# Kernel tuning notes

Measured on AMD Instinct MI355X. Metric: run time of the kernel, lower is better.

Reference implementation:

```python
import jax, jax.numpy as jnp
import numpy as np

B, C_IN, H, W = 4, 128, 32, 128   # W must equal out_channels (fc_out acts on last dim)
C_OUT, NUM_HEADS = 128, 2
BN_EPS = 1e-5


def setup_inputs() -> dict:
    key = jax.random.key(0)
    ks = jax.random.split(key, 14)
    s = 0.05  # small init scale for weights
    d = {
        "x": jax.random.normal(ks[0], (B, C_IN, H, W), jnp.float32),
        "wq": jax.random.normal(ks[1], (C_OUT, C_IN), jnp.float32) * s,
        "bq": jax.random.normal(ks[2], (C_OUT,), jnp.float32) * s,
        "wk": jax.random.normal(ks[3], (C_OUT, C_IN), jnp.float32) * s,
        "bk": jax.random.normal(ks[4], (C_OUT,), jnp.float32) * s,
        "wv": jax.random.normal(ks[5], (C_OUT, C_IN), jnp.float32) * s,
        "bv": jax.random.normal(ks[6], (C_OUT,), jnp.float32) * s,
        "fc_w": jax.random.normal(ks[7], (C_OUT, C_OUT), jnp.float32) * s,
        "fc_b": jax.random.normal(ks[8], (C_OUT,), jnp.float32) * s,
        "bn_gamma": jnp.ones((C_OUT,), jnp.float32),
        "bn_beta": jnp.zeros((C_OUT,), jnp.float32),
        "bn_mean": jax.random.normal(ks[9], (C_OUT,), jnp.float32) * 0.1,
        "bn_var": jax.random.uniform(ks[10], (C_OUT,), jnp.float32, 0.5, 1.5),
        "prelu_a": jnp.full((1,), 0.25, jnp.float32),
    }
    return d


def reference(x, wq, bq, wk, bk, wv, bv, fc_w, fc_b,
              bn_gamma, bn_beta, bn_mean, bn_var, prelu_a):
    b, c_in, h, w = x.shape
    c_out = wq.shape[0]
    nh = NUM_HEADS
    dk = c_out // nh
    L = h * w
    xf = x.reshape(b, c_in, L)                                # (B, Cin, L)
    # 1x1 convs == per-token linear projections
    q = jnp.einsum('oi,bil->bol', wq, xf) + bq[:, None]       # (B, Cout, L)
    k = jnp.einsum('oi,bil->bol', wk, xf) + bk[:, None]
    v = jnp.einsum('oi,bil->bol', wv, xf) + bv[:, None]
    Q = q.reshape(b, nh, dk, L)                               # (B, h, d_k, L)
    K = k.reshape(b, nh, dk, L)
    V = v.reshape(b, nh, dk, L)
    # scaled dot-product attention over the L = H*W tokens
    scores = jnp.einsum('bhdl,bhdm->bhlm', Q, K) / jnp.sqrt(jnp.float32(dk))
    attn = jax.nn.softmax(scores, axis=-1)                    # (B, h, L, L)
    out = jnp.einsum('bhlm,bhdm->bhdl', attn, V)              # (B, h, d_k, L)
    out = out.reshape(b, c_out, h, w)                         # (B, Cout, H, W)
    # fc_out: torch Linear on the LAST dim (W == Cout)
    y = jnp.einsum('bchw,ow->bcho', out, fc_w) + fc_b         # (B, Cout, H, W)
    # BatchNorm2d (eval mode: running stats) over channel dim
    inv = jax.lax.rsqrt(bn_var + BN_EPS)
    y = (y - bn_mean[None, :, None, None]) * (inv * bn_gamma)[None, :, None, None] \
        + bn_beta[None, :, None, None]
    # PReLU (single shared slope); dropout is identity in eval
    y = jnp.where(y > 0, y, prelu_a[0] * y)
    return y
```

## Files before the change

### kernel.cpp

```cpp
#include <hip/hip_runtime.h>

typedef _Float16 f16x8 __attribute__((ext_vector_type(8)));
typedef _Float16 f16x4t __attribute__((ext_vector_type(4)));
typedef __fp16 h16x2 __attribute__((ext_vector_type(2)));
typedef float f32x4 __attribute__((ext_vector_type(4)));
typedef float f32x16 __attribute__((ext_vector_type(16)));

#define L_SZ 4096

__device__ __forceinline__ unsigned short f2h(float f) {
    _Float16 h = (_Float16)f;
    return __builtin_bit_cast(unsigned short, h);
}
__device__ __forceinline__ unsigned int pk2(float a, float b) {
    h16x2 p = __builtin_amdgcn_cvt_pkrtz(a, b);
    return __builtin_bit_cast(unsigned int, p);
}

#define SLOT(row, ci) ((((ci) * 64) + ((row) & 32) + (((row) & 31) ^ (ci))) * 8)

__global__ __launch_bounds__(256, 1) void qkv_kernel(
    const float* __restrict__ x,
    const float* __restrict__ wq, const float* __restrict__ bq,
    const float* __restrict__ wk, const float* __restrict__ bk,
    const float* __restrict__ wv, const float* __restrict__ bv,
    unsigned short* __restrict__ Qp, unsigned short* __restrict__ Kp,
    unsigned short* __restrict__ Vp)
{
    int blk = blockIdx.x;
    int bidx = blk >> 6;
    int l0 = (blk & 63) * 64;
    int tid = threadIdx.x;
    int wave = tid >> 6, lane = tid & 63;
    int c = lane & 15, qd = lane >> 4;

    __shared__ __align__(16) unsigned short Ws[384 * 128];
    __shared__ __align__(16) unsigned short Sc[9216];

    #pragma unroll
    for (int t = 0; t < 96; ++t) {
        int e2 = tid + t * 256;
        const float* src = (e2 < 8192) ? wq : (e2 < 16384 ? wk : wv);
        int eo = (e2 * 2) & 16383;
        float2 v = *(const float2*)&src[eo];
        int e = e2 * 2;
        int o = e >> 7, ci = (e & 127) >> 3, j = e & 7;
        *(unsigned int*)&Ws[o * 128 + ((ci ^ (o & 15)) * 8) + j] = pk2(v.x, v.y);
    }

    unsigned short* Xs = Sc;
    #pragma unroll
    for (int it = 0; it < 8; ++it) {
        int i  = (tid >> 4) + 16 * it;
        int l4 = (tid & 15) * 4;
        const float4 v = *(const float4*)&x[(bidx * 128 + i) * L_SZ + l0 + l4];
        float vv[4] = {v.x, v.y, v.z, v.w};
        int ci = i >> 3;
        #pragma unroll
        for (int u = 0; u < 4; ++u) {
            int l = l4 + u;
            Xs[l * 128 + ((ci ^ (l & 15)) * 8) + (i & 7)] = f2h(vv[u]);
        }
    }
    __syncthreads();

    f16x8 afrag[4];
    #pragma unroll
    for (int kc = 0; kc < 4; ++kc) {
        int l = wave * 16 + c;
        int ci = kc * 4 + qd;
        afrag[kc] = *(const f16x8*)&Xs[l * 128 + ((ci ^ (l & 15)) * 8)];
    }
    __syncthreads();

    f32x4 acc[24];
    #pragma unroll
    for (int nt = 0; nt < 24; ++nt) acc[nt] = (f32x4){0.f, 0.f, 0.f, 0.f};

    #pragma unroll
    for (int kc = 0; kc < 4; ++kc) {
        #pragma unroll
        for (int nt = 0; nt < 24; ++nt) {
            int o = nt * 16 + c;
            f16x8 bfrag = *(const f16x8*)&Ws[o * 128 + (((kc * 4 + qd) ^ c) * 8)];
            acc[nt] = __builtin_amdgcn_mfma_f32_16x16x32_f16(afrag[kc], bfrag, acc[nt], 0, 0, 0);
        }
    }

    unsigned short* Vt = Sc;
    const float s_q = 0.18033688011f;
    #pragma unroll
    for (int nt = 0; nt < 24; ++nt) {
        int p = nt >> 3;
        int o = (nt & 7) * 16 + c;
        int h = o >> 6, d = o & 63;
        #pragma unroll
        for (int r = 0; r < 4; ++r) {
            int ll = wave * 16 + qd * 4 + r;
            int l = l0 + ll;
            float val = acc[nt][r];
            if (p == 0) {
                val = (val + bq[o]) * s_q;
                Qp[((bidx * 2 + h) * L_SZ + l) * 64 + d] = f2h(val);
            } else if (p == 1) {
                val += bk[o];
                Kp[((bidx * 2 + h) * L_SZ + l) * 64 + d] = f2h(val);
            } else {
                val += bv[o];
                Vt[o * 72 + ll] = f2h(val);
            }
        }
    }
    __syncthreads();
    #pragma unroll
    for (int t = 0; t < 2; ++t) {
        int u = tid + t * 256;
        int row = u >> 2;
        int lc = (u & 3) * 16;
        uint4 a0 = *(const uint4*)&Vt[row * 72 + lc];
        uint4 a1 = *(const uint4*)&Vt[row * 72 + lc + 8];
        *(uint4*)&Vp[(size_t)(bidx * 128 + row) * L_SZ + l0 + lc] = a0;
        *(uint4*)&Vp[(size_t)(bidx * 128 + row) * L_SZ + l0 + lc + 8] = a1;
    }
}

__global__ __launch_bounds__(256, 3) void attn_kernel(
    const unsigned short* __restrict__ Qp, const unsigned short* __restrict__ Kp,
    const unsigned short* __restrict__ Vp,
    unsigned short* __restrict__ Opart, float* __restrict__ Mpart, float* __restrict__ Lpart)
{
    int blk = blockIdx.x;
    int lt = blk & 31;
    int bh = (blk >> 5) & 7;
    int sp = blk >> 8;
    int l0 = lt * 128;
    int tid = threadIdx.x;
    int wave = tid >> 6, lane = tid & 63;
    int ln = lane & 31, hi = lane >> 5;
    int b = bh >> 1, h = bh & 1;

    __shared__ __align__(16) unsigned short Ks[2][4096];
    __shared__ __align__(16) unsigned short Vs[2][4096];
    __shared__ __align__(16) unsigned short Ps[4][2048];

    const unsigned short* Qb = Qp + (size_t)bh * L_SZ * 64;
    const unsigned short* Kb = Kp + (size_t)bh * L_SZ * 64;
    const unsigned short* Vb = Vp + ((size_t)b * 128 + h * 64) * L_SZ;

    int lq = l0 + wave * 32 + ln;
    f16x8 qf[4];
    #pragma unroll
    for (int kc = 0; kc < 4; ++kc)
        qf[kc] = *(const f16x8*)&Qb[(size_t)lq * 64 + kc * 16 + hi * 8];

    float m_st = -1e30f, lsum = 0.f;
    f32x16 acc0 = {}, acc1 = {};

    int urow = tid >> 3, uci = tid & 7;
    int mglob = sp * 1024;

    uint4 kreg[2], vreg[2];
    #pragma unroll
    for (int j = 0; j < 2; ++j) {
        int row = urow + j * 32;
        kreg[j] = *(const uint4*)&Kb[(size_t)(mglob + row) * 64 + uci * 8];
        vreg[j] = *(const uint4*)&Vb[(size_t)row * L_SZ + mglob + uci * 8];
    }
    #pragma unroll
    for (int j = 0; j < 2; ++j) {
        int row = urow + j * 32;
        *(uint4*)&Ks[0][SLOT(row, uci)] = kreg[j];
        *(uint4*)&Vs[0][SLOT(row, uci)] = vreg[j];
    }

    for (int it = 0; it < 16; ++it) {
        int cur = it & 1;
        __syncthreads();
        if (it < 15) {
            int m0 = mglob + (it + 1) * 64;
            #pragma unroll
            for (int j = 0; j < 2; ++j) {
                int row = urow + j * 32;
                kreg[j] = *(const uint4*)&Kb[(size_t)(m0 + row) * 64 + uci * 8];
                vreg[j] = *(const uint4*)&Vb[(size_t)row * L_SZ + m0 + uci * 8];
            }
        }

        f32x16 s0 = {}, s1 = {};
        #pragma unroll
        for (int kc = 0; kc < 4; ++kc) {
            int cd = kc * 2 + hi;
            f16x8 k0 = *(const f16x8*)&Ks[cur][SLOT(ln, cd)];
            f16x8 k1 = *(const f16x8*)&Ks[cur][SLOT(32 + ln, cd)];
            s0 = __builtin_amdgcn_mfma_f32_32x32x16_f16(k0, qf[kc], s0, 0, 0, 0);
            s1 = __builtin_amdgcn_mfma_f32_32x32x16_f16(k1, qf[kc], s1, 0, 0, 0);
        }

        float mx = s0[0];
        #pragma unroll
        for (int r = 1; r < 16; ++r) mx = fmaxf(mx, s0[r]);
        #pragma unroll
        for (int r = 0; r < 16; ++r) mx = fmaxf(mx, s1[r]);
        mx = fmaxf(mx, __shfl_xor(mx, 32));
        float mnew = fmaxf(m_st, mx);
        float alpha = exp2f(m_st - mnew);
        m_st = mnew;
        float rsum = 0.f;
        #pragma unroll
        for (int r = 0; r < 16; ++r) { float p = exp2f(s0[r] - mnew); s0[r] = p; rsum += p; }
        #pragma unroll
        for (int r = 0; r < 16; ++r) { float p = exp2f(s1[r] - mnew); s1[r] = p; rsum += p; }
        lsum = lsum * alpha + rsum;
        #pragma unroll
        for (int r = 0; r < 16; ++r) { acc0[r] *= alpha; acc1[r] *= alpha; }

        #pragma unroll
        for (int g = 0; g < 4; ++g) {
            uint2 w0;
            w0.x = pk2(s0[g * 4 + 0], s0[g * 4 + 1]);
            w0.y = pk2(s0[g * 4 + 2], s0[g * 4 + 3]);
            *(uint2*)&Ps[wave][(g * 32 + (ln ^ g)) * 8 + hi * 4] = w0;
            int g2 = 4 + g;
            uint2 w1;
            w1.x = pk2(s1[g * 4 + 0], s1[g * 4 + 1]);
            w1.y = pk2(s1[g * 4 + 2], s1[g * 4 + 3]);
            *(uint2*)&Ps[wave][(g2 * 32 + (ln ^ g2)) * 8 + hi * 4] = w1;
        }

        #pragma unroll
        for (int kc = 0; kc < 4; ++kc) {
            int cd = kc * 2 + hi;
            f16x8 pf = *(const f16x8*)&Ps[wave][(cd * 32 + (ln ^ cd)) * 8];
            f16x8 v0 = *(const f16x8*)&Vs[cur][SLOT(ln, cd)];
            f16x8 v1 = *(const f16x8*)&Vs[cur][SLOT(32 + ln, cd)];
            acc0 = __builtin_amdgcn_mfma_f32_32x32x16_f16(v0, pf, acc0, 0, 0, 0);
            acc1 = __builtin_amdgcn_mfma_f32_32x32x16_f16(v1, pf, acc1, 0, 0, 0);
        }

        if (it < 15) {
            #pragma unroll
            for (int j = 0; j < 2; ++j) {
                int row = urow + j * 32;
                *(uint4*)&Ks[cur ^ 1][SLOT(row, uci)] = kreg[j];
                *(uint4*)&Vs[cur ^ 1][SLOT(row, uci)] = vreg[j];
            }
        }
    }

    float l_tot = lsum + __shfl_xor(lsum, 32);
    unsigned short* Ow = Opart + (size_t)(sp * 8 + bh) * 64 * 4096;
    #pragma unroll
    for (int r = 0; r < 16; ++r) {
        int d0 = (r & 3) + 8 * (r >> 2) + 4 * hi;
        Ow[(size_t)d0 * 4096 + lq] = f2h(acc0[r]);
        Ow[(size_t)(32 + d0) * 4096 + lq] = f2h(acc1[r]);
    }
    if (hi == 0) {
        Mpart[(sp * 8 + bh) * 4096 + lq] = m_st;
        Lpart[(sp * 8 + bh) * 4096 + lq] = l_tot;
    }
}

__global__ __launch_bounds__(256, 1) void fc_kernel(
    const unsigned short* __restrict__ Opart, const float* __restrict__ Mp,
    const float* __restrict__ Lp, const float* __restrict__ fcw_f,
    const float* __restrict__ fc_b, const float* __restrict__ bn_g,
    const float* __restrict__ bn_b, const float* __restrict__ bn_m,
    const float* __restrict__ bn_v, const float* __restrict__ prelu_a,
    float* __restrict__ out)
{
    int blk = blockIdx.x;
    int r0 = blk * 64;
    int tid = threadIdx.x;
    int c0 = (r0 >> 5) & 127;
    int bh = (r0 >> 12) * 2 + (c0 >> 6);

    __shared__ __align__(16) unsigned short Fw[128 * 128];
    __shared__ __align__(16) unsigned short SclU[4096 * 4];

    #pragma unroll
    for (int t = 0; t < 16; ++t) {
        int l = tid + t * 256;
        float m0 = Mp[(0 * 8 + bh) * 4096 + l], m1 = Mp[(1 * 8 + bh) * 4096 + l];
        float m2 = Mp[(2 * 8 + bh) * 4096 + l], m3 = Mp[(3 * 8 + bh) * 4096 + l];
        float mx = fmaxf(fmaxf(m0, m1), fmaxf(m2, m3));
        float a0 = exp2f(m0 - mx), a1 = exp2f(m1 - mx);
        float a2 = exp2f(m2 - mx), a3 = exp2f(m3 - mx);
        float den = a0 * Lp[(0 * 8 + bh) * 4096 + l] + a1 * Lp[(1 * 8 + bh) * 4096 + l]
                  + a2 * Lp[(2 * 8 + bh) * 4096 + l] + a3 * Lp[(3 * 8 + bh) * 4096 + l];
        float inv = 1.0f / den;
        int hh = l >> 7, ww = l & 127;
        int slot = hh * 128 + ((ww + hh) & 127);
        uint2 sc;
        sc.x = pk2(a0 * inv, a1 * inv);
        sc.y = pk2(a2 * inv, a3 * inv);
        *(uint2*)&SclU[slot * 4] = sc;
    }
    #pragma unroll
    for (int t = 0; t < 32; ++t) {
        int e2 = tid + t * 256;
        float2 v = *(const float2*)&fcw_f[e2 * 2];
        int e = e2 * 2;
        int o = e >> 7, ci = (e & 127) >> 3, j = e & 7;
        *(unsigned int*)&Fw[o * 128 + ((ci ^ (o & 15)) * 8) + j] = pk2(v.x, v.y);
    }
    __syncthreads();

    int wave = tid >> 6, lane = tid & 63;
    int c = lane & 15, qd = lane >> 4;
    int rw = r0 + wave * 16;
    int row = rw + c;
    int ch = (row >> 5) & 127, hh = row & 31, d = ch & 63;

    f16x8 af[4];
    #pragma unroll
    for (int kc = 0; kc < 4; ++kc) {
        int w0 = kc * 32 + qd * 8;
        f16x8 ov[4];
        #pragma unroll
        for (int s = 0; s < 4; ++s)
            ov[s] = *(const f16x8*)&Opart[(size_t)(s * 8 + bh) * 262144 + (size_t)d * 4096 + hh * 128 + w0];
        #pragma unroll
        for (int j = 0; j < 8; ++j) {
            int slot = hh * 128 + ((w0 + j + hh) & 127);
            f16x4t sc = *(const f16x4t*)&SclU[slot * 4];
            float v = (float)ov[0][j] * (float)sc[0] + (float)ov[1][j] * (float)sc[1]
                    + (float)ov[2][j] * (float)sc[2] + (float)ov[3][j] * (float)sc[3];
            af[kc][j] = (_Float16)v;
        }
    }

    f32x4 acc[8];
    #pragma unroll
    for (int nt = 0; nt < 8; ++nt) acc[nt] = (f32x4){0.f, 0.f, 0.f, 0.f};
    #pragma unroll
    for (int kc = 0; kc < 4; ++kc) {
        #pragma unroll
        for (int nt = 0; nt < 8; ++nt) {
            int o = nt * 16 + c;
            f16x8 bf = *(const f16x8*)&Fw[o * 128 + (((kc * 4 + qd) ^ c) * 8)];
            acc[nt] = __builtin_amdgcn_mfma_f32_16x16x32_f16(af[kc], bf, acc[nt], 0, 0, 0);
        }
    }

    float pa = prelu_a[0];
    #pragma unroll
    for (int r = 0; r < 4; ++r) {
        int orow = rw + qd * 4 + r;
        int chn = (orow >> 5) & 127;
        float g  = bn_g[chn] * rsqrtf(bn_v[chn] + 1e-5f);
        float mn = bn_m[chn], bt = bn_b[chn];
        #pragma unroll
        for (int nt = 0; nt < 8; ++nt) {
            int o = nt * 16 + c;
            float y = (acc[nt][r] + fc_b[o] - mn) * g + bt;
            y = y > 0.f ? y : pa * y;
            out[(size_t)orow * 128 + o] = y;
        }
    }
}

extern "C" void kernel_launch(void* const* d_in, const int* in_sizes, int n_in,
                              void* d_out, int out_size, void* d_ws, size_t ws_size,
                              hipStream_t stream) {
    const float* x     = (const float*)d_in[0];
    const float* wq    = (const float*)d_in[1];
    const float* bq    = (const float*)d_in[2];
    const float* wk    = (const float*)d_in[3];
    const float* bk    = (const float*)d_in[4];
    const float* wv    = (const float*)d_in[5];
    const float* bv    = (const float*)d_in[6];
    const float* fcw_f = (const float*)d_in[7];
    const float* fcb   = (const float*)d_in[8];
    const float* bn_g  = (const float*)d_in[9];
    const float* bn_b  = (const float*)d_in[10];
    const float* bn_m  = (const float*)d_in[11];
    const float* bn_v  = (const float*)d_in[12];
    const float* pa    = (const float*)d_in[13];
    float* out = (float*)d_out;

    unsigned short* Qp  = (unsigned short*)d_ws;
    unsigned short* Kp  = Qp + 8 * L_SZ * 64;
    unsigned short* Vp  = Kp + 8 * L_SZ * 64;
    unsigned short* Opart = Vp + 8 * L_SZ * 64;
    float* Mpart = (float*)(Opart + 4 * 8 * 64 * L_SZ);
    float* Lpart = Mpart + 4 * 8 * L_SZ;

    hipLaunchKernelGGL(qkv_kernel,  dim3(256),  dim3(256), 0, stream,
                       x, wq, bq, wk, bk, wv, bv, Qp, Kp, Vp);
    hipLaunchKernelGGL(attn_kernel, dim3(1024), dim3(256), 0, stream,
                       Qp, Kp, Vp, Opart, Mpart, Lpart);
    hipLaunchKernelGGL(fc_kernel,   dim3(256),  dim3(256), 0, stream,
                       Opart, Mpart, Lpart, fcw_f, fcb, bn_g, bn_b, bn_m, bn_v, pa, out);
}
```

Before: 170.1 us.

## Split QKV and FC work across more blocks, single-buffer attention LDS, lazy rescale

```diff
diff --git a/kernel.cpp b/kernel.cpp
--- a/kernel.cpp
+++ b/kernel.cpp
@@ -16,10 +16,18 @@
     h16x2 p = __builtin_amdgcn_cvt_pkrtz(a, b);
     return __builtin_bit_cast(unsigned int, p);
 }
+__device__ __forceinline__ f16x8 ld8f(const float* __restrict__ p) {
+    float4 a = *(const float4*)p;
+    float4 b = *(const float4*)(p + 4);
+    uint4 u;
+    u.x = pk2(a.x, a.y); u.y = pk2(a.z, a.w);
+    u.z = pk2(b.x, b.y); u.w = pk2(b.z, b.w);
+    return __builtin_bit_cast(f16x8, u);
+}
 
 #define SLOT(row, ci) ((((ci) * 64) + ((row) & 32) + (((row) & 31) ^ (ci))) * 8)
 
-__global__ __launch_bounds__(256, 1) void qkv_kernel(
+__global__ __launch_bounds__(256) void qkv_kernel(
     const float* __restrict__ x,
     const float* __restrict__ wq, const float* __restrict__ bq,
     const float* __restrict__ wk, const float* __restrict__ bk,
@@ -28,27 +36,20 @@
     unsigned short* __restrict__ Vp)
 {
     int blk = blockIdx.x;
-    int bidx = blk >> 6;
-    int l0 = (blk & 63) * 64;
+    int proj = blk >> 8;
+    int rem = blk & 255;
+    int bidx = rem >> 6;
+    int l0 = (rem & 63) * 64;
     int tid = threadIdx.x;
     int wave = tid >> 6, lane = tid & 63;
     int c = lane & 15, qd = lane >> 4;
 
-    __shared__ __align__(16) unsigned short Ws[384 * 128];
-    __shared__ __align__(16) unsigned short Sc[9216];
-
-    #pragma unroll
-    for (int t = 0; t < 96; ++t) {
-        int e2 = tid + t * 256;
-        const float* src = (e2 < 8192) ? wq : (e2 < 16384 ? wk : wv);
-        int eo = (e2 * 2) & 16383;
-        float2 v = *(const float2*)&src[eo];
-        int e = e2 * 2;
-        int o = e >> 7, ci = (e & 127) >> 3, j = e & 7;
-        *(unsigned int*)&Ws[o * 128 + ((ci ^ (o & 15)) * 8) + j] = pk2(v.x, v.y);
-    }
-
-    unsigned short* Xs = Sc;
+    const float* W   = (proj == 0) ? wq : (proj == 1 ? wk : wv);
+    const float* bia = (proj == 0) ? bq : (proj == 1 ? bk : bv);
+
+    __shared__ __align__(16) unsigned short Sh[8448];
+
+    unsigned short* Xs = Sh;
     #pragma unroll
     for (int it = 0; it < 8; ++it) {
         int i  = (tid >> 4) + 16 * it;
@@ -73,58 +74,64 @@
     }
     __syncthreads();
 
-    f32x4 acc[24];
-    #pragma unroll
-    for (int nt = 0; nt < 24; ++nt) acc[nt] = (f32x4){0.f, 0.f, 0.f, 0.f};
+    f32x4 acc[8];
+    #pragma unroll
+    for (int nt = 0; nt < 8; ++nt) acc[nt] = (f32x4){0.f, 0.f, 0.f, 0.f};
 
     #pragma unroll
     for (int kc = 0; kc < 4; ++kc) {
         #pragma unroll
-        for (int nt = 0; nt < 24; ++nt) {
+        for (int nt = 0; nt < 8; ++nt) {
             int o = nt * 16 + c;
-            f16x8 bfrag = *(const f16x8*)&Ws[o * 128 + (((kc * 4 + qd) ^ c) * 8)];
+            f16x8 bfrag = ld8f(&W[o * 128 + kc * 32 + qd * 8]);
             acc[nt] = __builtin_amdgcn_mfma_f32_16x16x32_f16(afrag[kc], bfrag, acc[nt], 0, 0, 0);
         }
     }
 
-    unsigned short* Vt = Sc;
     const float s_q = 0.18033688011f;
-    #pragma unroll
-    for (int nt = 0; nt < 24; ++nt) {
-        int p = nt >> 3;
-        int o = (nt & 7) * 16 + c;
-        int h = o >> 6, d = o & 63;
-        #pragma unroll
-        for (int r = 0; r < 4; ++r) {
-            int ll = wave * 16 + qd * 4 + r;
-            int l = l0 + ll;
-            float val = acc[nt][r];
-            if (p == 0) {
-                val = (val + bq[o]) * s_q;
-                Qp[((bidx * 2 + h) * L_SZ + l) * 64 + d] = f2h(val);
-            } else if (p == 1) {
-                val += bk[o];
-                Kp[((bidx * 2 + h) * L_SZ + l) * 64 + d] = f2h(val);
-            } else {
-                val += bv[o];
-                Vt[o * 72 + ll] = f2h(val);
+    if (proj < 2) {
+        unsigned short* dst = (proj == 0) ? Qp : Kp;
+        #pragma unroll
+        for (int nt = 0; nt < 8; ++nt) {
+            int o = nt * 16 + c;
+            int h = o >> 6, d = o & 63;
+            float bo = bia[o];
+            #pragma unroll
+            for (int r = 0; r < 4; ++r) {
+                int l = l0 + wave * 16 + qd * 4 + r;
+                float val = acc[nt][r] + bo;
+                if (proj == 0) val *= s_q;
+                dst[((bidx * 2 + h) * L_SZ + l) * 64 + d] = f2h(val);
             }
         }
-    }
-    __syncthreads();
-    #pragma unroll
-    for (int t = 0; t < 2; ++t) {
-        int u = tid + t * 256;
-        int row = u >> 2;
-        int lc = (u & 3) * 16;
-        uint4 a0 = *(const uint4*)&Vt[row * 72 + lc];
-        uint4 a1 = *(const uint4*)&Vt[row * 72 + lc + 8];
-        *(uint4*)&Vp[(size_t)(bidx * 128 + row) * L_SZ + l0 + lc] = a0;
-        *(uint4*)&Vp[(size_t)(bidx * 128 + row) * L_SZ + l0 + lc + 8] = a1;
-    }
-}
-
-__global__ __launch_bounds__(256, 3) void attn_kernel(
+    } else {
+        unsigned short* Vt = Sh;
+        #pragma unroll
+        for (int nt = 0; nt < 8; ++nt) {
+            int o = nt * 16 + c;
+            float bo = bia[o];
+            #pragma unroll
+            for (int r = 0; r < 4; ++r) {
+                int ll = wave * 16 + qd * 4 + r;
+                Vt[o * 66 + ll] = f2h(acc[nt][r] + bo);
+            }
+        }
+        __syncthreads();
+        int row = tid >> 1;
+        int seg = (tid & 1) * 32;
+        #pragma unroll
+        for (int k = 0; k < 4; ++k) {
+            uint4 a;
+            a.x = *(unsigned int*)&Vt[row * 66 + seg + k * 8 + 0];
+            a.y = *(unsigned int*)&Vt[row * 66 + seg + k * 8 + 2];
+            a.z = *(unsigned int*)&Vt[row * 66 + seg + k * 8 + 4];
+            a.w = *(unsigned int*)&Vt[row * 66 + seg + k * 8 + 6];
+            *(uint4*)&Vp[(size_t)(bidx * 128 + row) * L_SZ + l0 + seg + k * 8] = a;
+        }
+    }
+}
+
+__global__ __launch_bounds__(256, 4) void attn_kernel(
     const unsigned short* __restrict__ Qp, const unsigned short* __restrict__ Kp,
     const unsigned short* __restrict__ Vp,
     unsigned short* __restrict__ Opart, float* __restrict__ Mpart, float* __restrict__ Lpart)
@@ -139,8 +146,8 @@
     int ln = lane & 31, hi = lane >> 5;
     int b = bh >> 1, h = bh & 1;
 
-    __shared__ __align__(16) unsigned short Ks[2][4096];
-    __shared__ __align__(16) unsigned short Vs[2][4096];
+    __shared__ __align__(16) unsigned short Ks[4096];
+    __shared__ __align__(16) unsigned short Vs[4096];
     __shared__ __align__(16) unsigned short Ps[4][2048];
 
     const unsigned short* Qb = Qp + (size_t)bh * L_SZ * 64;
@@ -166,16 +173,15 @@
         kreg[j] = *(const uint4*)&Kb[(size_t)(mglob + row) * 64 + uci * 8];
         vreg[j] = *(const uint4*)&Vb[(size_t)row * L_SZ + mglob + uci * 8];
     }
-    #pragma unroll
-    for (int j = 0; j < 2; ++j) {
-        int row = urow + j * 32;
-        *(uint4*)&Ks[0][SLOT(row, uci)] = kreg[j];
-        *(uint4*)&Vs[0][SLOT(row, uci)] = vreg[j];
-    }
 
     for (int it = 0; it < 16; ++it) {
-        int cur = it & 1;
         __syncthreads();
+        #pragma unroll
+        for (int j = 0; j < 2; ++j) {
+            int row = urow + j * 32;
+            *(uint4*)&Ks[SLOT(row, uci)] = kreg[j];
+            *(uint4*)&Vs[SLOT(row, uci)] = vreg[j];
+        }
         if (it < 15) {
             int m0 = mglob + (it + 1) * 64;
             #pragma unroll
@@ -185,13 +191,14 @@
                 vreg[j] = *(const uint4*)&Vb[(size_t)row * L_SZ + m0 + uci * 8];
             }
         }
+        __syncthreads();
 
         f32x16 s0 = {}, s1 = {};
         #pragma unroll
         for (int kc = 0; kc < 4; ++kc) {
             int cd = kc * 2 + hi;
-            f16x8 k0 = *(const f16x8*)&Ks[cur][SLOT(ln, cd)];
-            f16x8 k1 = *(const f16x8*)&Ks[cur][SLOT(32 + ln, cd)];
+            f16x8 k0 = *(const f16x8*)&Ks[SLOT(ln, cd)];
+            f16x8 k1 = *(const f16x8*)&Ks[SLOT(32 + ln, cd)];
             s0 = __builtin_amdgcn_mfma_f32_32x32x16_f16(k0, qf[kc], s0, 0, 0, 0);
             s1 = __builtin_amdgcn_mfma_f32_32x32x16_f16(k1, qf[kc], s1, 0, 0, 0);
         }
@@ -202,17 +209,20 @@
         #pragma unroll
         for (int r = 0; r < 16; ++r) mx = fmaxf(mx, s1[r]);
         mx = fmaxf(mx, __shfl_xor(mx, 32));
-        float mnew = fmaxf(m_st, mx);
-        float alpha = exp2f(m_st - mnew);
-        m_st = mnew;
+        if (__any(mx > m_st)) {
+            float mnew = fmaxf(m_st, mx);
+            float alpha = exp2f(m_st - mnew);
+            m_st = mnew;
+            lsum *= alpha;
+            #pragma unroll
+            for (int r = 0; r < 16; ++r) { acc0[r] *= alpha; acc1[r] *= alpha; }
+        }
         float rsum = 0.f;
         #pragma unroll
-        for (int r = 0; r < 16; ++r) { float p = exp2f(s0[r] - mnew); s0[r] = p; rsum += p; }
-        #pragma unroll
-        for (int r = 0; r < 16; ++r) { float p = exp2f(s1[r] - mnew); s1[r] = p; rsum += p; }
-        lsum = lsum * alpha + rsum;
-        #pragma unroll
-        for (int r = 0; r < 16; ++r) { acc0[r] *= alpha; acc1[r] *= alpha; }
+        for (int r = 0; r < 16; ++r) { float p = exp2f(s0[r] - m_st); s0[r] = p; rsum += p; }
+        #pragma unroll
+        for (int r = 0; r < 16; ++r) { float p = exp2f(s1[r] - m_st); s1[r] = p; rsum += p; }
+        lsum += rsum;
 
         #pragma unroll
         for (int g = 0; g < 4; ++g) {
@@ -231,19 +241,10 @@
         for (int kc = 0; kc < 4; ++kc) {
             int cd = kc * 2 + hi;
             f16x8 pf = *(const f16x8*)&Ps[wave][(cd * 32 + (ln ^ cd)) * 8];
-            f16x8 v0 = *(const f16x8*)&Vs[cur][SLOT(ln, cd)];
-            f16x8 v1 = *(const f16x8*)&Vs[cur][SLOT(32 + ln, cd)];
+            f16x8 v0 = *(const f16x8*)&Vs[SLOT(ln, cd)];
+            f16x8 v1 = *(const f16x8*)&Vs[SLOT(32 + ln, cd)];
             acc0 = __builtin_amdgcn_mfma_f32_32x32x16_f16(v0, pf, acc0, 0, 0, 0);
             acc1 = __builtin_amdgcn_mfma_f32_32x32x16_f16(v1, pf, acc1, 0, 0, 0);
-        }
-
-        if (it < 15) {
-            #pragma unroll
-            for (int j = 0; j < 2; ++j) {
-                int row = urow + j * 32;
-                *(uint4*)&Ks[cur ^ 1][SLOT(row, uci)] = kreg[j];
-                *(uint4*)&Vs[cur ^ 1][SLOT(row, uci)] = vreg[j];
-            }
         }
     }
 
@@ -261,56 +262,43 @@
     }
 }
 
-__global__ __launch_bounds__(256, 1) void fc_kernel(
-    const unsigned short* __restrict__ Opart, const float* __restrict__ Mp,
-    const float* __restrict__ Lp, const float* __restrict__ fcw_f,
-    const float* __restrict__ fc_b, const float* __restrict__ bn_g,
-    const float* __restrict__ bn_b, const float* __restrict__ bn_m,
-    const float* __restrict__ bn_v, const float* __restrict__ prelu_a,
-    float* __restrict__ out)
+__global__ __launch_bounds__(256) void scale_kernel(
+    const float* __restrict__ Mp, const float* __restrict__ Lp,
+    unsigned short* __restrict__ Scl)
+{
+    int t = blockIdx.x * 256 + threadIdx.x;
+    float m[4], l[4];
+    #pragma unroll
+    for (int s = 0; s < 4; ++s) { m[s] = Mp[s * 32768 + t]; l[s] = Lp[s * 32768 + t]; }
+    float mx = fmaxf(fmaxf(m[0], m[1]), fmaxf(m[2], m[3]));
+    float a[4], den = 0.f;
+    #pragma unroll
+    for (int s = 0; s < 4; ++s) { a[s] = exp2f(m[s] - mx); den += a[s] * l[s]; }
+    float inv = 1.0f / den;
+    uint2 sc;
+    sc.x = pk2(a[0] * inv, a[1] * inv);
+    sc.y = pk2(a[2] * inv, a[3] * inv);
+    *(uint2*)&Scl[t * 4] = sc;
+}
+
+__global__ __launch_bounds__(128) void fc_kernel(
+    const unsigned short* __restrict__ Opart, const unsigned short* __restrict__ Scl,
+    const float* __restrict__ fcw_f, const float* __restrict__ fc_b,
+    const float* __restrict__ bn_g, const float* __restrict__ bn_b,
+    const float* __restrict__ bn_m, const float* __restrict__ bn_v,
+    const float* __restrict__ prelu_a, float* __restrict__ out)
 {
     int blk = blockIdx.x;
-    int r0 = blk * 64;
+    int ch = blk & 127;
+    int bh = (blk >> 7) * 2 + (ch >> 6);
+    int d = ch & 63;
     int tid = threadIdx.x;
-    int c0 = (r0 >> 5) & 127;
-    int bh = (r0 >> 12) * 2 + (c0 >> 6);
-
-    __shared__ __align__(16) unsigned short Fw[128 * 128];
-    __shared__ __align__(16) unsigned short SclU[4096 * 4];
-
-    #pragma unroll
-    for (int t = 0; t < 16; ++t) {
-        int l = tid + t * 256;
-        float m0 = Mp[(0 * 8 + bh) * 4096 + l], m1 = Mp[(1 * 8 + bh) * 4096 + l];
-        float m2 = Mp[(2 * 8 + bh) * 4096 + l], m3 = Mp[(3 * 8 + bh) * 4096 + l];
-        float mx = fmaxf(fmaxf(m0, m1), fmaxf(m2, m3));
-        float a0 = exp2f(m0 - mx), a1 = exp2f(m1 - mx);
-        float a2 = exp2f(m2 - mx), a3 = exp2f(m3 - mx);
-        float den = a0 * Lp[(0 * 8 + bh) * 4096 + l] + a1 * Lp[(1 * 8 + bh) * 4096 + l]
-                  + a2 * Lp[(2 * 8 + bh) * 4096 + l] + a3 * Lp[(3 * 8 + bh) * 4096 + l];
-        float inv = 1.0f / den;
-        int hh = l >> 7, ww = l & 127;
-        int slot = hh * 128 + ((ww + hh) & 127);
-        uint2 sc;
-        sc.x = pk2(a0 * inv, a1 * inv);
-        sc.y = pk2(a2 * inv, a3 * inv);
-        *(uint2*)&SclU[slot * 4] = sc;
-    }
-    #pragma unroll
-    for (int t = 0; t < 32; ++t) {
-        int e2 = tid + t * 256;
-        float2 v = *(const float2*)&fcw_f[e2 * 2];
-        int e = e2 * 2;
-        int o = e >> 7, ci = (e & 127) >> 3, j = e & 7;
-        *(unsigned int*)&Fw[o * 128 + ((ci ^ (o & 15)) * 8) + j] = pk2(v.x, v.y);
-    }
-    __syncthreads();
-
     int wave = tid >> 6, lane = tid & 63;
     int c = lane & 15, qd = lane >> 4;
-    int rw = r0 + wave * 16;
-    int row = rw + c;
-    int ch = (row >> 5) & 127, hh = row & 31, d = ch & 63;
+    int hh = wave * 16 + c;
+
+    size_t obase = (size_t)bh * 262144 + (size_t)d * 4096 + hh * 128;
+    int sbase = (bh << 12) + hh * 128;
 
     f16x8 af[4];
     #pragma unroll
@@ -319,11 +307,10 @@
         f16x8 ov[4];
         #pragma unroll
         for (int s = 0; s < 4; ++s)
-            ov[s] = *(const f16x8*)&Opart[(size_t)(s * 8 + bh) * 262144 + (size_t)d * 4096 + hh * 128 + w0];
+            ov[s] = *(const f16x8*)&Opart[(size_t)s * 2097152 + obase + w0];
         #pragma unroll
         for (int j = 0; j < 8; ++j) {
-            int slot = hh * 128 + ((w0 + j + hh) & 127);
-            f16x4t sc = *(const f16x4t*)&SclU[slot * 4];
+            f16x4t sc = *(const f16x4t*)&Scl[(sbase + w0 + j) * 4];
             float v = (float)ov[0][j] * (float)sc[0] + (float)ov[1][j] * (float)sc[1]
                     + (float)ov[2][j] * (float)sc[2] + (float)ov[3][j] * (float)sc[3];
             af[kc][j] = (_Float16)v;
@@ -337,19 +324,18 @@
     for (int kc = 0; kc < 4; ++kc) {
         #pragma unroll
         for (int nt = 0; nt < 8; ++nt) {
-            int o = nt * 16 + c;
-            f16x8 bf = *(const f16x8*)&Fw[o * 128 + (((kc * 4 + qd) ^ c) * 8)];
+            f16x8 bf = ld8f(&fcw_f[(nt * 16 + c) * 128 + kc * 32 + qd * 8]);
             acc[nt] = __builtin_amdgcn_mfma_f32_16x16x32_f16(af[kc], bf, acc[nt], 0, 0, 0);
         }
     }
 
     float pa = prelu_a[0];
+    float g  = bn_g[ch] * rsqrtf(bn_v[ch] + 1e-5f);
+    float mn = bn_m[ch], bt = bn_b[ch];
+    int rbase = blk * 32 + wave * 16;
     #pragma unroll
     for (int r = 0; r < 4; ++r) {
-        int orow = rw + qd * 4 + r;
-        int chn = (orow >> 5) & 127;
-        float g  = bn_g[chn] * rsqrtf(bn_v[chn] + 1e-5f);
-        float mn = bn_m[chn], bt = bn_b[chn];
+        int orow = rbase + qd * 4 + r;
         #pragma unroll
         for (int nt = 0; nt < 8; ++nt) {
             int o = nt * 16 + c;
@@ -385,11 +371,14 @@
     unsigned short* Opart = Vp + 8 * L_SZ * 64;
     float* Mpart = (float*)(Opart + 4 * 8 * 64 * L_SZ);
     float* Lpart = Mpart + 4 * 8 * L_SZ;
-
-    hipLaunchKernelGGL(qkv_kernel,  dim3(256),  dim3(256), 0, stream,
+    unsigned short* Scl = (unsigned short*)(Lpart + 4 * 8 * L_SZ);
+
+    hipLaunchKernelGGL(qkv_kernel,   dim3(768),  dim3(256), 0, stream,
                        x, wq, bq, wk, bk, wv, bv, Qp, Kp, Vp);
-    hipLaunchKernelGGL(attn_kernel, dim3(1024), dim3(256), 0, stream,
+    hipLaunchKernelGGL(attn_kernel,  dim3(1024), dim3(256), 0, stream,
                        Qp, Kp, Vp, Opart, Mpart, Lpart);
-    hipLaunchKernelGGL(fc_kernel,   dim3(256),  dim3(256), 0, stream,
-                       Opart, Mpart, Lpart, fcw_f, fcb, bn_g, bn_b, bn_m, bn_v, pa, out);
-}
+    hipLaunchKernelGGL(scale_kernel, dim3(128),  dim3(256), 0, stream,
+                       Mpart, Lpart, Scl);
+    hipLaunchKernelGGL(fc_kernel,    dim3(512),  dim3(128), 0, stream,
+                       Opart, Scl, fcw_f, fcb, bn_g, bn_b, bn_m, bn_v, pa, out);
+}
```

Measured after the change: 216.6 us. 1.27x slower.
